# Optimization experiments

Hardware: AMD Instinct MI355X
Metric: run time of the kernel (lower is better)

The kernel has to match this reference:

```python
import jax, jax.numpy as jnp
import numpy as np
import math

D_MODEL = 1024
N_HEADS = 16
D_K = D_MODEL // N_HEADS
B, S = 2, 2048


def setup_inputs() -> dict:
    key = jax.random.key(0)
    ks = jax.random.split(key, 11)
    sc = 1.0 / math.sqrt(D_MODEL)
    inp = {
        'q': jax.random.normal(ks[0], (B, S, D_MODEL), jnp.float32),
        'k': jax.random.normal(ks[1], (B, S, D_MODEL), jnp.float32),
        'v': jax.random.normal(ks[2], (B, S, D_MODEL), jnp.float32),
        'mask': jnp.tril(jnp.ones((S, S), jnp.int32))[None, None],  # [1,1,S,S] causal
        'W_q': jax.random.normal(ks[3], (D_MODEL, D_MODEL), jnp.float32) * sc,
        'b_q': jnp.zeros((D_MODEL,), jnp.float32),
        'W_k': jax.random.normal(ks[4], (D_MODEL, D_MODEL), jnp.float32) * sc,
        'b_k': jnp.zeros((D_MODEL,), jnp.float32),
        'W_v': jax.random.normal(ks[5], (D_MODEL, D_MODEL), jnp.float32) * sc,
        'b_v': jnp.zeros((D_MODEL,), jnp.float32),
        'W_o': jax.random.normal(ks[6], (D_MODEL, D_MODEL), jnp.float32) * sc,
        'b_o': jnp.zeros((D_MODEL,), jnp.float32),
    }
    return inp


def reference(q, k, v, mask, W_q, b_q, W_k, b_k, W_v, b_v, W_o, b_o):
    # Linear projections then split heads: [B,S,D] -> [B,H,S,d_k]
    def split_heads(x):
        b, s, _ = x.shape
        return x.reshape(b, s, N_HEADS, D_K).transpose(0, 2, 1, 3)

    Q = split_heads(q @ W_q + b_q)
    K = split_heads(k @ W_k + b_k)
    V = split_heads(v @ W_v + b_v)

    scores = jnp.einsum('bhqd,bhkd->bhqk', Q, K) / math.sqrt(D_K)
    scores = jnp.where(mask == 0, jnp.float32(-1e9), scores)
    attn = jax.nn.softmax(scores, axis=-1)  # dropout is identity in eval mode
    out = jnp.einsum('bhqk,bhkd->bhqd', attn, V)
    out = out.transpose(0, 2, 1, 3).reshape(q.shape[0], -1, D_MODEL)
    return out @ W_o + b_o
```

## Files before the change

kernel.cpp:

```cpp
#include <hip/hip_runtime.h>
#include <hip/hip_bf16.h>

#define D_MODEL 1024
#define S_LEN   2048
#define BATCH   2
#define NH      16
#define DK      64

typedef __bf16 bf16_t;
typedef __attribute__((ext_vector_type(8))) __bf16 bf16x8;
typedef __attribute__((ext_vector_type(4))) float f32x4;

#if __has_builtin(__builtin_amdgcn_exp2f)
#define EXP2F(x) __builtin_amdgcn_exp2f(x)
#else
#define EXP2F(x) exp2f(x)
#endif

#define Q_SCALE 0.1803368801111204f

#define GLDS16(gp, lp) __builtin_amdgcn_global_load_lds( \
    (const __attribute__((address_space(1))) void*)(gp), \
    (__attribute__((address_space(3))) void*)(lp), 16, 0, 0)

__global__ void prep_w(const float* __restrict__ Wq, const float* __restrict__ Wk,
                       const float* __restrict__ Wv, const float* __restrict__ Wo,
                       bf16_t* __restrict__ WqkvT, bf16_t* __restrict__ WoT)
{
    __shared__ float t[32][33];
    const int mat = blockIdx.z;
    const int tile = blockIdx.x;
    const int bx = tile & 31, by = tile >> 5;
    const float* in = (mat == 0) ? Wq : (mat == 1) ? Wk : (mat == 2) ? Wv : Wo;
    bf16_t* out = (mat < 3) ? (WqkvT + (long)mat * D_MODEL * D_MODEL) : WoT;
    int tx = threadIdx.x, ty = threadIdx.y;
    int gx = bx * 32, gy = by * 32;
#pragma unroll
    for (int i = 0; i < 32; i += 8)
        t[ty + i][tx] = in[(gy + ty + i) * D_MODEL + gx + tx];
    __syncthreads();
#pragma unroll
    for (int i = 0; i < 32; i += 8)
        out[(gx + ty + i) * D_MODEL + gy + tx] = (bf16_t)t[tx][ty + i];
}

#define BN 128
#define BKT 64

template <int ROWS>
__device__ __forceinline__ void stage_swz(const bf16_t* __restrict__ G, int row0,
                                          int k0, bf16_t* __restrict__ Ls, int tid) {
#pragma unroll
    for (int it = 0; it < ROWS / 32; ++it) {
        int g = it * 256 + tid;
        int row = g >> 3;
        int c = (g & 7) ^ (row & 7);
        GLDS16(&G[(long)(row0 + row) * D_MODEL + k0 + c * 8],
               &Ls[(it * 256 + (tid & ~63)) * 8]);
    }
}

__device__ __forceinline__ bf16x8 frag_swz(const bf16_t* __restrict__ Ls, int row, int cg) {
    return *(const bf16x8*)(&Ls[(row * 8 + (cg ^ (row & 7))) * 8]);
}

__device__ __forceinline__ bf16x8 cvt8(float4 a, float4 b) {
    bf16x8 o;
    o[0] = (bf16_t)a.x; o[1] = (bf16_t)a.y; o[2] = (bf16_t)a.z; o[3] = (bf16_t)a.w;
    o[4] = (bf16_t)b.x; o[5] = (bf16_t)b.y; o[6] = (bf16_t)b.z; o[7] = (bf16_t)b.w;
    return o;
}

#define QM 64
constexpr int QKV_SMEM = (QM * BKT + BN * BKT);
__global__ __launch_bounds__(256) void gemm_qkv(
    const float* __restrict__ qsrc, const float* __restrict__ ksrc,
    const float* __restrict__ vsrc, const bf16_t* __restrict__ WqkvT,
    const float* __restrict__ bq, const float* __restrict__ bk, const float* __restrict__ bv,
    bf16_t* __restrict__ Qw, bf16_t* __restrict__ Kw, bf16_t* __restrict__ Vt)
{
    __shared__ __align__(16) bf16_t smem[QKV_SMEM];
    bf16_t* As = smem;
    bf16_t* Bs = smem + QM * BKT;
    const int z = blockIdx.z;
    const float* A   = (z == 0) ? qsrc : (z == 1) ? ksrc : vsrc;
    const bf16_t* BT = WqkvT + (long)z * D_MODEL * D_MODEL;
    const float* bias = (z == 0) ? bq : (z == 1) ? bk : bv;
    bf16_t* Cb = (z == 0) ? Qw : (z == 1) ? Kw : Vt;
    const float oscale = (z == 0) ? Q_SCALE : 1.0f;

    const int tid  = threadIdx.x;
    const int wave = tid >> 6, lane = tid & 63;
    const int lrow = lane & 15, kgrp = lane >> 4;
    const int wm = (wave >> 1) * 32, wn = (wave & 1) * 64;
    int lin = blockIdx.y * 8 + blockIdx.x;
    int m0 = (lin & 63) * QM;
    int n0 = (lin >> 6) * BN;

    const int ar0 = tid >> 3,        ac0 = tid & 7;
    const int ar1 = (256 + tid) >> 3, ac1 = tid & 7;
    const int as0 = (ar0 * 8 + (ac0 ^ (ar0 & 7))) * 8;
    const int as1 = (ar1 * 8 + (ac1 ^ (ar1 & 7))) * 8;
    const float* arow0 = &A[(long)(m0 + ar0) * D_MODEL + ac0 * 8];
    const float* arow1 = &A[(long)(m0 + ar1) * D_MODEL + ac1 * 8];

    float4 pa0a = *(const float4*)(arow0);
    float4 pa0b = *(const float4*)(arow0 + 4);
    float4 pa1a = *(const float4*)(arow1);
    float4 pa1b = *(const float4*)(arow1 + 4);

    f32x4 acc[2][4] = {};

    for (int k0 = 0; k0 < D_MODEL; k0 += BKT) {
        __syncthreads();
        stage_swz<BN>(BT, n0, k0, Bs, tid);
        *(bf16x8*)(&As[as0]) = cvt8(pa0a, pa0b);
        *(bf16x8*)(&As[as1]) = cvt8(pa1a, pa1b);
        __syncthreads();
        if (k0 + BKT < D_MODEL) {
            pa0a = *(const float4*)(arow0 + k0 + BKT);
            pa0b = *(const float4*)(arow0 + k0 + BKT + 4);
            pa1a = *(const float4*)(arow1 + k0 + BKT);
            pa1b = *(const float4*)(arow1 + k0 + BKT + 4);
        }
#pragma unroll
        for (int kk = 0; kk < 2; ++kk) {
            bf16x8 af[2], bfr[4];
#pragma unroll
            for (int mi = 0; mi < 2; ++mi)
                af[mi] = frag_swz(As, wm + mi * 16 + lrow, kk * 4 + kgrp);
#pragma unroll
            for (int ni = 0; ni < 4; ++ni)
                bfr[ni] = frag_swz(Bs, wn + ni * 16 + lrow, kk * 4 + kgrp);
#pragma unroll
            for (int mi = 0; mi < 2; ++mi)
#pragma unroll
                for (int ni = 0; ni < 4; ++ni)
                    acc[mi][ni] = __builtin_amdgcn_mfma_f32_16x16x32_bf16(af[mi], bfr[ni], acc[mi][ni], 0, 0, 0);
        }
    }

    if (z != 2) {
#pragma unroll
        for (int mi = 0; mi < 2; ++mi)
#pragma unroll
            for (int ni = 0; ni < 4; ++ni) {
                int col = n0 + wn + ni * 16 + lrow;
                float bvf = bias[col];
#pragma unroll
                for (int r = 0; r < 4; ++r) {
                    int row = m0 + wm + mi * 16 + kgrp * 4 + r;
                    float vv = (acc[mi][ni][r] + bvf) * oscale;
                    int b = row >> 11, s = row & (S_LEN - 1);
                    int h = col >> 6, d = col & (DK - 1);
                    Cb[(((long)(b * NH + h) * S_LEN + s) * DK) + d] = (bf16_t)vv;
                }
            }
    } else {
        bf16_t* Ct = smem;
        __syncthreads();
#pragma unroll
        for (int mi = 0; mi < 2; ++mi)
#pragma unroll
            for (int ni = 0; ni < 4; ++ni) {
                int cl = wn + ni * 16 + lrow;
                float bvf = bias[n0 + cl];
#pragma unroll
                for (int r = 0; r < 4; ++r) {
                    int rl = wm + mi * 16 + kgrp * 4 + r;
                    Ct[cl * 72 + rl] = (bf16_t)(acc[mi][ni][r] + bvf);
                }
            }
        __syncthreads();
        const int b = m0 >> 11, sbase = m0 & (S_LEN - 1);
#pragma unroll
        for (int pass = 0; pass < 4; ++pass) {
            int dl = pass * 32 + (tid >> 3);
            int sc = (tid & 7) * 8;
            int colg = n0 + dl;
            int h = colg >> 6, d = colg & (DK - 1);
            bf16_t* dst = Cb + (((long)(b * NH + h) * DK + d) * S_LEN + sbase + sc);
            *(bf16x8*)(dst) = *(const bf16x8*)&Ct[dl * 72 + sc];
        }
    }
}

#define OM 64
__global__ __launch_bounds__(256) void gemm_out(
    const bf16_t* __restrict__ A, const bf16_t* __restrict__ BT,
    const float* __restrict__ bias, float* __restrict__ Cf)
{
    __shared__ __align__(16) bf16_t As[OM * BKT];
    __shared__ __align__(16) bf16_t Bs[BN * BKT];
    const int tid  = threadIdx.x;
    const int wave = tid >> 6, lane = tid & 63;
    const int lrow = lane & 15, kgrp = lane >> 4;
    const int wm = (wave >> 1) * 32, wn = (wave & 1) * 64;
    int lin = blockIdx.y * 8 + blockIdx.x;
    int m0 = (lin & 63) * OM;
    int n0 = (lin >> 6) * BN;

    f32x4 acc[2][4] = {};

    for (int k0 = 0; k0 < D_MODEL; k0 += BKT) {
        stage_swz<OM>(A, m0, k0, As, tid);
        stage_swz<BN>(BT, n0, k0, Bs, tid);
        __syncthreads();
#pragma unroll
        for (int kk = 0; kk < 2; ++kk) {
            bf16x8 af[2], bfr[4];
#pragma unroll
            for (int mi = 0; mi < 2; ++mi)
                af[mi] = frag_swz(As, wm + mi * 16 + lrow, kk * 4 + kgrp);
#pragma unroll
            for (int ni = 0; ni < 4; ++ni)
                bfr[ni] = frag_swz(Bs, wn + ni * 16 + lrow, kk * 4 + kgrp);
#pragma unroll
            for (int mi = 0; mi < 2; ++mi)
#pragma unroll
                for (int ni = 0; ni < 4; ++ni)
                    acc[mi][ni] = __builtin_amdgcn_mfma_f32_16x16x32_bf16(af[mi], bfr[ni], acc[mi][ni], 0, 0, 0);
        }
        __syncthreads();
    }

#pragma unroll
    for (int mi = 0; mi < 2; ++mi)
#pragma unroll
        for (int ni = 0; ni < 4; ++ni) {
            int col = n0 + wn + ni * 16 + lrow;
            float bvf = bias[col];
#pragma unroll
            for (int r = 0; r < 4; ++r) {
                int row = m0 + wm + mi * 16 + kgrp * 4 + r;
                Cf[(long)row * D_MODEL + col] = acc[mi][ni][r] + bvf;
            }
        }
}

__device__ __forceinline__ int krow_perm(int r) {
    return ((r >> 5) + 2 * ((r >> 2) & 1)) * 16 + ((r >> 3) & 3) * 4 + (r & 3);
}

__device__ __forceinline__ void attn_one_qtile(
    int qi, int bh, int wave, int lrow, int kgrp,
    int r0, int c0, int r1,
    const bf16_t* __restrict__ Qh, const bf16_t* __restrict__ Kh,
    const bf16_t* __restrict__ Vth, bf16_t* __restrict__ O,
    bf16_t* __restrict__ Ks, bf16_t* __restrict__ Vs)
{
    const int q0 = qi * 64;
    const int qrow = q0 + wave * 16;
    const int qg = qrow + lrow;

    bf16x8 qf[2];
#pragma unroll
    for (int kk = 0; kk < 2; ++kk)
        qf[kk] = *(const bf16x8*)(&Qh[(qrow + lrow) * DK + kk * 32 + kgrp * 8]);

    f32x4 acc[4] = {};
    float lsum = 0.f;

    const int nt = qi + 1;
    const int rr0 = krow_perm(r0), rr1 = krow_perm(r1);

    uint4 kpre0 = *(const uint4*)(&Kh[(long)r0 * DK + c0]);
    uint4 kpre1 = *(const uint4*)(&Kh[(long)r1 * DK + c0]);
    uint4 vpre0 = *(const uint4*)(&Vth[(long)r0 * S_LEN + c0]);
    uint4 vpre1 = *(const uint4*)(&Vth[(long)r1 * S_LEN + c0]);

    for (int t = 0; t < nt; ++t) {
        __syncthreads();
        *(uint4*)(&Ks[rr0 * 72 + c0]) = kpre0;
        *(uint4*)(&Ks[rr1 * 72 + c0]) = kpre1;
        *(uint4*)(&Vs[r0 * 72 + c0]) = vpre0;
        *(uint4*)(&Vs[r1 * 72 + c0]) = vpre1;
        if (t + 1 < nt) {
            const int j0n = (t + 1) * 64;
            kpre0 = *(const uint4*)(&Kh[(long)(j0n + r0) * DK + c0]);
            kpre1 = *(const uint4*)(&Kh[(long)(j0n + r1) * DK + c0]);
            vpre0 = *(const uint4*)(&Vth[(long)r0 * S_LEN + j0n + c0]);
            vpre1 = *(const uint4*)(&Vth[(long)r1 * S_LEN + j0n + c0]);
        }
        __syncthreads();

        const int j0 = t * 64;

        f32x4 sc[4] = {};
#pragma unroll
        for (int kk = 0; kk < 2; ++kk)
#pragma unroll
            for (int ni = 0; ni < 4; ++ni) {
                bf16x8 kf = *(const bf16x8*)(&Ks[(ni * 16 + lrow) * 72 + kk * 32 + kgrp * 8]);
                sc[ni] = __builtin_amdgcn_mfma_f32_16x16x32_bf16(kf, qf[kk], sc[ni], 0, 0, 0);
            }

        float pb[4][4];
        const bool needmask = (j0 + 63 > qrow);
        if (needmask) {
#pragma unroll
            for (int ni = 0; ni < 4; ++ni) {
                const int cb = j0 + (ni & 1) * 32 + kgrp * 8 + ((ni >> 1) << 2);
#pragma unroll
                for (int r = 0; r < 4; ++r) {
                    float pv = EXP2F(sc[ni][r]);
                    if (cb + r > qg) pv = 0.f;
                    lsum += pv;
                    pb[ni][r] = pv;
                }
            }
        } else {
#pragma unroll
            for (int ni = 0; ni < 4; ++ni)
#pragma unroll
                for (int r = 0; r < 4; ++r) {
                    float pv = EXP2F(sc[ni][r]);
                    lsum += pv;
                    pb[ni][r] = pv;
                }
        }

        bf16x8 pf0, pf1;
#pragma unroll
        for (int r = 0; r < 4; ++r) {
            pf0[r]     = (bf16_t)pb[0][r];
            pf0[r + 4] = (bf16_t)pb[2][r];
            pf1[r]     = (bf16_t)pb[1][r];
            pf1[r + 4] = (bf16_t)pb[3][r];
        }

#pragma unroll
        for (int di = 0; di < 4; ++di) {
            bf16x8 vf = *(const bf16x8*)(&Vs[(di * 16 + lrow) * 72 + kgrp * 8]);
            acc[di] = __builtin_amdgcn_mfma_f32_16x16x32_bf16(pf0, vf, acc[di], 0, 0, 0);
        }
#pragma unroll
        for (int di = 0; di < 4; ++di) {
            bf16x8 vf = *(const bf16x8*)(&Vs[(di * 16 + lrow) * 72 + 32 + kgrp * 8]);
            acc[di] = __builtin_amdgcn_mfma_f32_16x16x32_bf16(pf1, vf, acc[di], 0, 0, 0);
        }
    }

    lsum += __shfl_xor(lsum, 16);
    lsum += __shfl_xor(lsum, 32);

    const int b = bh >> 4, h = bh & (NH - 1);
#pragma unroll
    for (int r = 0; r < 4; ++r) {
        float inv = 1.f / __shfl(lsum, kgrp * 4 + r);
        int s = qrow + kgrp * 4 + r;
#pragma unroll
        for (int di = 0; di < 4; ++di) {
            int d = di * 16 + lrow;
            O[((long)(b * S_LEN + s)) * D_MODEL + h * DK + d] = (bf16_t)(acc[di][r] * inv);
        }
    }
}

__global__ __launch_bounds__(256, 2) void attn_kernel(
    const bf16_t* __restrict__ Q, const bf16_t* __restrict__ K,
    const bf16_t* __restrict__ Vt, bf16_t* __restrict__ O)
{
    __shared__ __align__(16) bf16_t Ks[64 * 72];
    __shared__ __align__(16) bf16_t Vs[64 * 72];

    const int bh = blockIdx.y;
    const int p  = blockIdx.x;
    const int tid = threadIdx.x, wave = tid >> 6, lane = tid & 63;
    const int lrow = lane & 15, kgrp = lane >> 4;

    const bf16_t* Qh  = Q  + (long)bh * S_LEN * DK;
    const bf16_t* Kh  = K  + (long)bh * S_LEN * DK;
    const bf16_t* Vth = Vt + (long)bh * DK * S_LEN;

    const int f0 = tid * 8;
    const int r0 = f0 >> 6, c0 = f0 & 63;
    const int r1 = (f0 + 2048) >> 6;

    attn_one_qtile(31 - p, bh, wave, lrow, kgrp, r0, c0, r1,
                   Qh, Kh, Vth, O, Ks, Vs);
    attn_one_qtile(p, bh, wave, lrow, kgrp, r0, c0, r1,
                   Qh, Kh, Vth, O, Ks, Vs);
}

extern "C" void kernel_launch(void* const* d_in, const int* in_sizes, int n_in,
                              void* d_out, int out_size, void* d_ws, size_t ws_size,
                              hipStream_t stream) {
    const float* q  = (const float*)d_in[0];
    const float* k  = (const float*)d_in[1];
    const float* v  = (const float*)d_in[2];
    const float* Wq = (const float*)d_in[4];
    const float* bq = (const float*)d_in[5];
    const float* Wk = (const float*)d_in[6];
    const float* bk = (const float*)d_in[7];
    const float* Wv = (const float*)d_in[8];
    const float* bv = (const float*)d_in[9];
    const float* Wo = (const float*)d_in[10];
    const float* bo = (const float*)d_in[11];

    char* ws = (char*)d_ws;
    const size_t Mi = 1024 * 1024;
    bf16_t* WqkvT = (bf16_t*)(ws);
    bf16_t* WoT   = (bf16_t*)(ws + 6 * Mi);
    bf16_t* Qw    = (bf16_t*)(ws + 8 * Mi);
    bf16_t* Kw    = (bf16_t*)(ws + 16 * Mi);
    bf16_t* Vtw   = (bf16_t*)(ws + 24 * Mi);
    bf16_t* Aw    = (bf16_t*)(ws + 32 * Mi);

    dim3 tb(32, 8);
    prep_w<<<dim3(1024, 1, 4), tb, 0, stream>>>(Wq, Wk, Wv, Wo, WqkvT, WoT);

    gemm_qkv<<<dim3(8, (BATCH * S_LEN) / QM, 3), 256, 0, stream>>>(
        q, k, v, WqkvT, bq, bk, bv, Qw, Kw, Vtw);

    attn_kernel<<<dim3(16, BATCH * NH), 256, 0, stream>>>(Qw, Kw, Vtw, Aw);

    gemm_out<<<dim3(8, (BATCH * S_LEN) / OM), 256, 0, stream>>>(
        Aw, WoT, bo, (float*)d_out);
}
```

Baseline: 217.6 us.

## Double-buffer attention K/V tiles with direct global-to-LDS loads and swizzled layout

Result: no change. 218.9 us (+0.6%).

```diff
diff --git a/kernel.cpp b/kernel.cpp
--- a/kernel.cpp
+++ b/kernel.cpp
@@ -97,7 +97,7 @@
     int m0 = (lin & 63) * QM;
     int n0 = (lin >> 6) * BN;
 
-    const int ar0 = tid >> 3,        ac0 = tid & 7;
+    const int ar0 = tid >> 3,         ac0 = tid & 7;
     const int ar1 = (256 + tid) >> 3, ac1 = tid & 7;
     const int as0 = (ar0 * 8 + (ac0 ^ (ar0 & 7))) * 8;
     const int as1 = (ar1 * 8 + (ac1 ^ (ar1 & 7))) * 8;
@@ -238,19 +238,37 @@
         }
 }
 
-__device__ __forceinline__ int krow_perm(int r) {
-    return ((r >> 5) + 2 * ((r >> 2) & 1)) * 16 + ((r >> 3) & 3) * 4 + (r & 3);
+__device__ __forceinline__ void stage_k(const bf16_t* __restrict__ Kt,
+                                        bf16_t* __restrict__ Ls, int tid) {
+#pragma unroll
+    for (int it = 0; it < 2; ++it) {
+        int g = it * 256 + tid;
+        int row = g >> 3;
+        int srow = 32 * ((row >> 4) & 1) + 8 * ((row >> 2) & 3)
+                 + 4 * (row >> 5) + (row & 3);
+        int c = (g & 7) ^ (row & 7);
+        GLDS16(&Kt[(long)srow * DK + c * 8], &Ls[(it * 256 + (tid & ~63)) * 8]);
+    }
+}
+
+__device__ __forceinline__ void stage_v(const bf16_t* __restrict__ Vth, int j0,
+                                        bf16_t* __restrict__ Ls, int tid) {
+#pragma unroll
+    for (int it = 0; it < 2; ++it) {
+        int g = it * 256 + tid;
+        int row = g >> 3;
+        int c = (g & 7) ^ (row & 7);
+        GLDS16(&Vth[(long)row * S_LEN + j0 + c * 8], &Ls[(it * 256 + (tid & ~63)) * 8]);
+    }
 }
 
 __device__ __forceinline__ void attn_one_qtile(
-    int qi, int bh, int wave, int lrow, int kgrp,
-    int r0, int c0, int r1,
+    int qi, int bh, int wave, int lrow, int kgrp, int tid,
     const bf16_t* __restrict__ Qh, const bf16_t* __restrict__ Kh,
     const bf16_t* __restrict__ Vth, bf16_t* __restrict__ O,
-    bf16_t* __restrict__ Ks, bf16_t* __restrict__ Vs)
+    bf16_t (*Ks)[64 * 64], bf16_t (*Vs)[64 * 64])
 {
-    const int q0 = qi * 64;
-    const int qrow = q0 + wave * 16;
+    const int qrow = qi * 64 + wave * 16;
     const int qg = qrow + lrow;
 
     bf16x8 qf[2];
@@ -262,28 +280,19 @@
     float lsum = 0.f;
 
     const int nt = qi + 1;
-    const int rr0 = krow_perm(r0), rr1 = krow_perm(r1);
-
-    uint4 kpre0 = *(const uint4*)(&Kh[(long)r0 * DK + c0]);
-    uint4 kpre1 = *(const uint4*)(&Kh[(long)r1 * DK + c0]);
-    uint4 vpre0 = *(const uint4*)(&Vth[(long)r0 * S_LEN + c0]);
-    uint4 vpre1 = *(const uint4*)(&Vth[(long)r1 * S_LEN + c0]);
+
+    stage_k(Kh, Ks[0], tid);
+    stage_v(Vth, 0, Vs[0], tid);
+    __syncthreads();
 
     for (int t = 0; t < nt; ++t) {
-        __syncthreads();
-        *(uint4*)(&Ks[rr0 * 72 + c0]) = kpre0;
-        *(uint4*)(&Ks[rr1 * 72 + c0]) = kpre1;
-        *(uint4*)(&Vs[r0 * 72 + c0]) = vpre0;
-        *(uint4*)(&Vs[r1 * 72 + c0]) = vpre1;
+        const int cur = t & 1;
         if (t + 1 < nt) {
-            const int j0n = (t + 1) * 64;
-            kpre0 = *(const uint4*)(&Kh[(long)(j0n + r0) * DK + c0]);
-            kpre1 = *(const uint4*)(&Kh[(long)(j0n + r1) * DK + c0]);
-            vpre0 = *(const uint4*)(&Vth[(long)r0 * S_LEN + j0n + c0]);
-            vpre1 = *(const uint4*)(&Vth[(long)r1 * S_LEN + j0n + c0]);
-        }
-        __syncthreads();
-
+            stage_k(Kh + (long)(t + 1) * 64 * DK, Ks[cur ^ 1], tid);
+            stage_v(Vth, (t + 1) * 64, Vs[cur ^ 1], tid);
+        }
+        const bf16_t* Kc = Ks[cur];
+        const bf16_t* Vc = Vs[cur];
         const int j0 = t * 64;
 
         f32x4 sc[4] = {};
@@ -291,7 +300,7 @@
         for (int kk = 0; kk < 2; ++kk)
 #pragma unroll
             for (int ni = 0; ni < 4; ++ni) {
-                bf16x8 kf = *(const bf16x8*)(&Ks[(ni * 16 + lrow) * 72 + kk * 32 + kgrp * 8]);
+                bf16x8 kf = frag_swz(Kc, ni * 16 + lrow, kk * 4 + kgrp);
                 sc[ni] = __builtin_amdgcn_mfma_f32_16x16x32_bf16(kf, qf[kk], sc[ni], 0, 0, 0);
             }
 
@@ -331,14 +340,16 @@
 
 #pragma unroll
         for (int di = 0; di < 4; ++di) {
-            bf16x8 vf = *(const bf16x8*)(&Vs[(di * 16 + lrow) * 72 + kgrp * 8]);
+            bf16x8 vf = frag_swz(Vc, di * 16 + lrow, kgrp);
             acc[di] = __builtin_amdgcn_mfma_f32_16x16x32_bf16(pf0, vf, acc[di], 0, 0, 0);
         }
 #pragma unroll
         for (int di = 0; di < 4; ++di) {
-            bf16x8 vf = *(const bf16x8*)(&Vs[(di * 16 + lrow) * 72 + 32 + kgrp * 8]);
+            bf16x8 vf = frag_swz(Vc, di * 16 + lrow, 4 + kgrp);
             acc[di] = __builtin_amdgcn_mfma_f32_16x16x32_bf16(pf1, vf, acc[di], 0, 0, 0);
         }
+
+        __syncthreads();
     }
 
     lsum += __shfl_xor(lsum, 16);
@@ -361,8 +372,8 @@
     const bf16_t* __restrict__ Q, const bf16_t* __restrict__ K,
     const bf16_t* __restrict__ Vt, bf16_t* __restrict__ O)
 {
-    __shared__ __align__(16) bf16_t Ks[64 * 72];
-    __shared__ __align__(16) bf16_t Vs[64 * 72];
+    __shared__ __align__(16) bf16_t Ks[2][64 * 64];
+    __shared__ __align__(16) bf16_t Vs[2][64 * 64];
 
     const int bh = blockIdx.y;
     const int p  = blockIdx.x;
@@ -373,13 +384,9 @@
     const bf16_t* Kh  = K  + (long)bh * S_LEN * DK;
     const bf16_t* Vth = Vt + (long)bh * DK * S_LEN;
 
-    const int f0 = tid * 8;
-    const int r0 = f0 >> 6, c0 = f0 & 63;
-    const int r1 = (f0 + 2048) >> 6;
-
-    attn_one_qtile(31 - p, bh, wave, lrow, kgrp, r0, c0, r1,
+    attn_one_qtile(31 - p, bh, wave, lrow, kgrp, tid,
                    Qh, Kh, Vth, O, Ks, Vs);
-    attn_one_qtile(p, bh, wave, lrow, kgrp, r0, c0, r1,
+    attn_one_qtile(p, bh, wave, lrow, kgrp, tid,
                    Qh, Kh, Vth, O, Ks, Vs);
 }
 
```
